# Kernel optimization log

Hardware: AMD Instinct MI355X
Metric: run time of the kernel (lower is better)

## Reference

```python
import jax, jax.numpy as jnp
import numpy as np

ALPHA = 0.1        # axis_aligned_projection threshold
NEG_INF = -1e30    # large negative used for masking (softmax-equivalent to -inf)


def axis_aligned_projection(x, alpha=ALPHA):
    x_abs = jnp.abs(x)
    max_vals = jnp.max(x_abs, axis=-1, keepdims=True)
    axis_weights = jnp.where(x_abs >= alpha * max_vals, x_abs, 0.0)
    return axis_weights * jnp.sign(x)


def setup_inputs() -> dict:
    key = jax.random.key(0)
    kq, kk, kv = jax.random.split(key, 3)
    B, L, H, E = 4, 2048, 8, 64
    S, D = L, E
    queries = jax.random.normal(kq, (B, L, H, E), dtype=jnp.float32)
    keys = jax.random.normal(kk, (B, S, H, E), dtype=jnp.float32)
    values = jax.random.normal(kv, (B, S, H, D), dtype=jnp.float32)
    # TriangularCausalMask: True strictly above the diagonal -> masked out
    causal = jnp.triu(jnp.ones((L, S), dtype=jnp.bool_), k=1)
    attn_mask = jnp.broadcast_to(causal[None, None], (B, 1, L, S))
    return {"queries": queries, "keys": keys, "values": values, "attn_mask": attn_mask}


def reference(queries, keys, values, attn_mask):
    B, L, H, E = queries.shape
    scale = 1.0 / jnp.sqrt(jnp.float32(E))
    q = axis_aligned_projection(queries)
    k = axis_aligned_projection(keys)
    # [B,H,L,S] dense scores (the module materializes the full matrix)
    scores = jnp.einsum('blhe,bshe->bhls', q, k)
    scores = jnp.where(attn_mask, NEG_INF, scores)
    A = jax.nn.softmax(scale * scores, axis=-1)  # dropout is identity in eval mode
    V = jnp.einsum('bhls,bshd->blhd', A, values)
    return V
```

## Files before the change

kernel.cpp:

```cpp
#include <hip/hip_runtime.h>
#include <hip/hip_bf16.h>
#include <stdint.h>

#define B_ 4
#define L_ 2048
#define H_ 8
#define E_ 64
#define ALPHA 0.1f
#define LOG2E 1.44269504088896f
#define QSCALE (0.125f * LOG2E)
#define KSTR 72

typedef float f32x4 __attribute__((ext_vector_type(4)));
typedef short bf16x8 __attribute__((ext_vector_type(8)));
typedef short bf16x4 __attribute__((ext_vector_type(4)));
typedef uint32_t u32;
typedef unsigned short u16;
typedef u32 u32x2 __attribute__((ext_vector_type(2)));

__device__ __forceinline__ u16 f2bf(float f) {
    u32 x = __builtin_bit_cast(u32, f);
    u32 r = x + 0x7fffu + ((x >> 16) & 1u);
    return (u16)(r >> 16);
}

__device__ __forceinline__ u32 pk2bf(float a, float b) {
    u32 ua = __builtin_bit_cast(u32, a) + 0x8000u;
    u32 ub = __builtin_bit_cast(u32, b) + 0x8000u;
    return (ua >> 16) | (ub & 0xffff0000u);
}

__device__ __forceinline__ f32x4 mfma16x16x16bf16(bf16x4 a, bf16x4 b, f32x4 c) {
#if __has_builtin(__builtin_amdgcn_mfma_f32_16x16x16bf16_1k)
    return __builtin_amdgcn_mfma_f32_16x16x16bf16_1k(a, b, c, 0, 0, 0);
#elif __has_builtin(__builtin_amdgcn_mfma_f32_16x16x16_bf16)
    return __builtin_amdgcn_mfma_f32_16x16x16_bf16(a, b, c, 0, 0, 0);
#else
    f32x4 d;
    asm volatile("v_mfma_f32_16x16x16_bf16 %0, %1, %2, %3"
                 : "=v"(d) : "v"(a), "v"(b), "v"(c));
    return d;
#endif
}

__device__ __forceinline__ void dma16(const u16* g, u16* l) {
    __builtin_amdgcn_global_load_lds(
        (const __attribute__((address_space(1))) void*)g,
        (__attribute__((address_space(3))) void*)l, 16, 0, 0);
}

__global__ __launch_bounds__(256) void prep_kernel(const float* __restrict__ qin,
                                                   const float* __restrict__ kin,
                                                   const float* __restrict__ vin,
                                                   u16* __restrict__ qp,
                                                   u16* __restrict__ kp,
                                                   u16* __restrict__ vt) {
    __shared__ u16 tile[64][66];
    if (blockIdx.x < 4096) {
        const int RG = (B_ * L_ * H_) / 8;
        int wave = threadIdx.x >> 6, lane = threadIdx.x & 63;
        int g = blockIdx.x * 4 + wave;
        const float* src;
        u16* dst;
        int gr, ostr;
        float sc;
        if (g < RG) { src = qin; dst = qp; gr = g; sc = QSCALE; ostr = 64; }
        else        { src = kin; dst = kp; gr = g - RG; sc = 1.0f; ostr = KSTR; }

        int rig = lane >> 3;
        int c = (lane & 7) * 4;
        int row = gr * 8 + rig;

        const float* rp = src + (size_t)row * 64;
        float4 v0 = *(const float4*)(rp + c);
        float4 v1 = *(const float4*)(rp + c + 32);
        float f[8] = {v0.x, v0.y, v0.z, v0.w, v1.x, v1.y, v1.z, v1.w};

        float mx = 0.f;
#pragma unroll
        for (int i = 0; i < 8; ++i) mx = fmaxf(mx, fabsf(f[i]));
#pragma unroll
        for (int m = 1; m < 8; m <<= 1) mx = fmaxf(mx, __shfl_xor(mx, m));
        float thr = ALPHA * mx;

        u16 o[8];
#pragma unroll
        for (int i = 0; i < 8; ++i)
            o[i] = (fabsf(f[i]) >= thr) ? f2bf(f[i] * sc) : (u16)0;

        int b = row >> 14;
        int l = (row >> 3) & (L_ - 1);
        int h = row & 7;
        u16* orow = dst + ((size_t)(b * H_ + h) * L_ + l) * ostr;
        uint2 p0 = {(u32)o[0] | ((u32)o[1] << 16), (u32)o[2] | ((u32)o[3] << 16)};
        uint2 p1 = {(u32)o[4] | ((u32)o[5] << 16), (u32)o[6] | ((u32)o[7] << 16)};
        *(uint2*)(orow + c) = p0;
        *(uint2*)(orow + c + 32) = p1;
    } else {
        int bx = blockIdx.x - 4096;
        int bh = bx >> 5, sblk = bx & 31;
        int b = bh >> 3, h = bh & 7;
        int t = threadIdx.x;
        int s0 = sblk * 64;

#pragma unroll
        for (int p = 0; p < 2; ++p) {
            int sl = p * 32 + (t >> 3);
            int c = (t & 7) * 4;
            const float* rp = vin + (((size_t)(b * L_ + s0 + sl)) * H_ + h) * 64;
            float4 a = *(const float4*)(rp + c);
            float4 bb = *(const float4*)(rp + c + 32);
            u32* d0 = (u32*)&tile[sl][c];
            d0[0] = (u32)f2bf(a.x) | ((u32)f2bf(a.y) << 16);
            d0[1] = (u32)f2bf(a.z) | ((u32)f2bf(a.w) << 16);
            u32* d1 = (u32*)&tile[sl][c + 32];
            d1[0] = (u32)f2bf(bb.x) | ((u32)f2bf(bb.y) << 16);
            d1[1] = (u32)f2bf(bb.z) | ((u32)f2bf(bb.w) << 16);
        }
        __syncthreads();
#pragma unroll
        for (int p = 0; p < 2; ++p) {
            int d = p * 32 + (t >> 3);
            int sc2 = (t & 7) * 8;
            u16 o[8];
#pragma unroll
            for (int i = 0; i < 8; ++i) o[i] = tile[sc2 + i][d];
            uint4 val;
            val.x = (u32)o[0] | ((u32)o[1] << 16);
            val.y = (u32)o[2] | ((u32)o[3] << 16);
            val.z = (u32)o[4] | ((u32)o[5] << 16);
            val.w = (u32)o[6] | ((u32)o[7] << 16);
            *(uint4*)(vt + ((size_t)(bh * 32 + sblk) * 64 + d) * KSTR + sc2) = val;
        }
    }
}

__global__ __launch_bounds__(256, 2) void flash_kernel(const u16* __restrict__ Qp,
                                                       const u16* __restrict__ Kp,
                                                       const u16* __restrict__ Vt,
                                                       float* __restrict__ out) {
    __shared__ u16 kbuf[2][64 * KSTR];
    __shared__ u16 vbuf[2][64 * KSTR];
    int t = threadIdx.x;
    int wave = t >> 6, lane = t & 63;
    int bh = blockIdx.x & 31;
    int j = blockIdx.x >> 5;
    int qg = (blockIdx.x < 256) ? (15 - j) : (j - 8);
    int lo = lane & 15, quad = lane >> 4;
    int b = bh >> 3, h = bh & 7;
    int qA = qg * 128 + wave * 16;
    int qB = qA + 64;
    int dA = qg * 2;
    int T = dA + 1;

    const u16* kTiles = Kp + (size_t)bh * L_ * KSTR;
    const u16* vTiles = Vt + (size_t)bh * 32 * 64 * KSTR;

    auto stage = [&](int sb, int buf) {
        const u16* kg = kTiles + (size_t)sb * KSTR;
        const u16* vg = vTiles + (size_t)(sb >> 6) * 64 * KSTR;
        u16* kl = kbuf[buf];
        u16* vl = vbuf[buf];
        for (int i = wave; i < 18; i += 4) {
            if (i < 9) dma16(kg + i * 512 + lane * 8, kl + i * 512);
            else       dma16(vg + (i - 9) * 512 + lane * 8, vl + (i - 9) * 512);
        }
    };

    const u16* qbA = Qp + ((size_t)bh * L_ + qA + lo) * 64 + quad * 8;
    bf16x8 aQA0 = *(const bf16x8*)(qbA);
    bf16x8 aQA1 = *(const bf16x8*)(qbA + 32);
    const u16* qbB = Qp + ((size_t)bh * L_ + qB + lo) * 64 + quad * 8;
    bf16x8 aQB0 = *(const bf16x8*)(qbB);
    bf16x8 aQB1 = *(const bf16x8*)(qbB + 32);

    f32x4 oA[4], oB[4];
#pragma unroll
    for (int ni = 0; ni < 4; ++ni) {
        oA[ni] = (f32x4){0.f, 0.f, 0.f, 0.f};
        oB[ni] = (f32x4){0.f, 0.f, 0.f, 0.f};
    }
    float lsA = 0.f, lsB = 0.f;

    auto frag_proc = [&](bf16x8 k0, bf16x8 k1, const bf16x4* vf,
                         bf16x8 fq0, bf16x8 fq1, f32x4* oacc, float& lsacc,
                         bool diag) {
        f32x4 S = {0.f, 0.f, 0.f, 0.f};
        S = __builtin_amdgcn_mfma_f32_16x16x32_bf16(k0, fq0, S, 0, 0, 0);
        S = __builtin_amdgcn_mfma_f32_16x16x32_bf16(k1, fq1, S, 0, 0, 0);
        float P[4];
#pragma unroll
        for (int r = 0; r < 4; ++r) {
            float e = __builtin_amdgcn_exp2f(S[r]);
            P[r] = (diag && (quad * 4 + r > lo)) ? 0.f : e;
        }
        lsacc += (P[0] + P[1]) + (P[2] + P[3]);
        u32x2 pk = {pk2bf(P[0], P[1]), pk2bf(P[2], P[3])};
        bf16x4 aP = __builtin_bit_cast(bf16x4, pk);
#pragma unroll
        for (int ni = 0; ni < 4; ++ni)
            oacc[ni] = mfma16x16x16bf16(aP, vf[ni], oacc[ni]);
    };

    stage(0, 0);
    __syncthreads();

    for (int kt = 0; kt < dA; ++kt) {
        int cur = kt & 1;
        stage((kt + 1) << 6, cur ^ 1);
        const u16* ks = kbuf[cur];
        const u16* vs = vbuf[cur];
#pragma unroll
        for (int sub = 0; sub < 4; ++sub) {
            bf16x8 k0 = *(const bf16x8*)(ks + (sub * 16 + lo) * KSTR + quad * 8);
            bf16x8 k1 = *(const bf16x8*)(ks + (sub * 16 + lo) * KSTR + 32 + quad * 8);
            bf16x4 vf[4];
#pragma unroll
            for (int ni = 0; ni < 4; ++ni)
                vf[ni] = *(const bf16x4*)(vs + (ni * 16 + lo) * KSTR + sub * 16 + quad * 4);
            frag_proc(k0, k1, vf, aQA0, aQA1, oA, lsA, false);
            frag_proc(k0, k1, vf, aQB0, aQB1, oB, lsB, false);
        }
        __syncthreads();
    }

    {
        int cur = dA & 1;
        stage(T << 6, cur ^ 1);
        const u16* ks = kbuf[cur];
        const u16* vs = vbuf[cur];
#pragma unroll
        for (int sub = 0; sub < 4; ++sub) {
            bf16x8 k0 = *(const bf16x8*)(ks + (sub * 16 + lo) * KSTR + quad * 8);
            bf16x8 k1 = *(const bf16x8*)(ks + (sub * 16 + lo) * KSTR + 32 + quad * 8);
            bf16x4 vf[4];
#pragma unroll
            for (int ni = 0; ni < 4; ++ni)
                vf[ni] = *(const bf16x4*)(vs + (ni * 16 + lo) * KSTR + sub * 16 + quad * 4);
            frag_proc(k0, k1, vf, aQB0, aQB1, oB, lsB, false);
            if (sub < wave)
                frag_proc(k0, k1, vf, aQA0, aQA1, oA, lsA, false);
            else if (sub == wave)
                frag_proc(k0, k1, vf, aQA0, aQA1, oA, lsA, true);
        }
        __syncthreads();
    }

    {
        int cur = T & 1;
        const u16* ks = kbuf[cur];
        const u16* vs = vbuf[cur];
        for (int sub = 0; sub <= wave; ++sub) {
            bf16x8 k0 = *(const bf16x8*)(ks + (sub * 16 + lo) * KSTR + quad * 8);
            bf16x8 k1 = *(const bf16x8*)(ks + (sub * 16 + lo) * KSTR + 32 + quad * 8);
            bf16x4 vf[4];
#pragma unroll
            for (int ni = 0; ni < 4; ++ni)
                vf[ni] = *(const bf16x4*)(vs + (ni * 16 + lo) * KSTR + sub * 16 + quad * 4);
            frag_proc(k0, k1, vf, aQB0, aQB1, oB, lsB, sub == wave);
        }
    }

    auto epi = [&](float ls, const f32x4* oacc, int q0f) {
        ls += __shfl_xor(ls, 16);
        ls += __shfl_xor(ls, 32);
#pragma unroll
        for (int r = 0; r < 4; ++r) {
            float lr = __shfl(ls, quad * 4 + r);
            float inv = 1.0f / lr;
            int q = q0f + quad * 4 + r;
            float* ob = out + (((size_t)(b * L_ + q)) * H_ + h) * 64 + lo;
            ob[0]  = oacc[0][r] * inv;
            ob[16] = oacc[1][r] * inv;
            ob[32] = oacc[2][r] * inv;
            ob[48] = oacc[3][r] * inv;
        }
    };
    epi(lsA, oA, qA);
    epi(lsB, oB, qB);
}

extern "C" void kernel_launch(void* const* d_in, const int* in_sizes, int n_in,
                              void* d_out, int out_size, void* d_ws, size_t ws_size,
                              hipStream_t stream) {
    const float* q = (const float*)d_in[0];
    const float* k = (const float*)d_in[1];
    const float* v = (const float*)d_in[2];
    float* out = (float*)d_out;

    const size_t QSZ = (size_t)B_ * H_ * L_ * 64;
    const size_t KSZ = (size_t)B_ * H_ * L_ * KSTR;
    u16* qp = (u16*)d_ws;
    u16* kp = qp + QSZ;
    u16* vt = kp + KSZ;

    prep_kernel<<<5120, 256, 0, stream>>>(q, k, v, qp, kp, vt);
    flash_kernel<<<512, 256, 0, stream>>>(qp, kp, vt, out);
}
```

Measured before the change: 172.9 us.

## Split 128-row query blocks into 64-row blocks and double grid size

Each block now handles 64 query rows (one 16-row fragment per wave) instead of two 16-row fragments per wave across 128 rows. The grid doubles to 1024 blocks, launch bounds rise to 4 blocks per CU, and the causal schedule is remapped so heavy and light blocks interleave. The aim is better occupancy and load balance. The cost is that each K/V tile staged in LDS is reused by half as many query rows, so LDS and global traffic go up.

```diff
diff --git a/kernel.cpp b/kernel.cpp
--- a/kernel.cpp
+++ b/kernel.cpp
@@ -135,7 +135,7 @@
     }
 }
 
-__global__ __launch_bounds__(256, 2) void flash_kernel(const u16* __restrict__ Qp,
+__global__ __launch_bounds__(256, 4) void flash_kernel(const u16* __restrict__ Qp,
                                                        const u16* __restrict__ Kp,
                                                        const u16* __restrict__ Vt,
                                                        float* __restrict__ out) {
@@ -144,14 +144,12 @@
     int t = threadIdx.x;
     int wave = t >> 6, lane = t & 63;
     int bh = blockIdx.x & 31;
-    int j = blockIdx.x >> 5;
-    int qg = (blockIdx.x < 256) ? (15 - j) : (j - 8);
+    int r5 = blockIdx.x >> 5;
+    int g = r5 & 7, kr = r5 >> 3;
+    int qq = (kr == 0) ? (31 - g) : (kr == 1) ? (16 + g) : (kr == 2) ? (15 - g) : g;
     int lo = lane & 15, quad = lane >> 4;
+    int q0 = qq * 64 + wave * 16;
     int b = bh >> 3, h = bh & 7;
-    int qA = qg * 128 + wave * 16;
-    int qB = qA + 64;
-    int dA = qg * 2;
-    int T = dA + 1;
 
     const u16* kTiles = Kp + (size_t)bh * L_ * KSTR;
     const u16* vTiles = Vt + (size_t)bh * 32 * 64 * KSTR;
@@ -167,117 +165,75 @@
         }
     };
 
-    const u16* qbA = Qp + ((size_t)bh * L_ + qA + lo) * 64 + quad * 8;
-    bf16x8 aQA0 = *(const bf16x8*)(qbA);
-    bf16x8 aQA1 = *(const bf16x8*)(qbA + 32);
-    const u16* qbB = Qp + ((size_t)bh * L_ + qB + lo) * 64 + quad * 8;
-    bf16x8 aQB0 = *(const bf16x8*)(qbB);
-    bf16x8 aQB1 = *(const bf16x8*)(qbB + 32);
-
-    f32x4 oA[4], oB[4];
-#pragma unroll
-    for (int ni = 0; ni < 4; ++ni) {
-        oA[ni] = (f32x4){0.f, 0.f, 0.f, 0.f};
-        oB[ni] = (f32x4){0.f, 0.f, 0.f, 0.f};
-    }
-    float lsA = 0.f, lsB = 0.f;
-
-    auto frag_proc = [&](bf16x8 k0, bf16x8 k1, const bf16x4* vf,
-                         bf16x8 fq0, bf16x8 fq1, f32x4* oacc, float& lsacc,
-                         bool diag) {
+    const u16* qbase = Qp + ((size_t)bh * L_ + q0 + lo) * 64 + quad * 8;
+    bf16x8 aQ0 = *(const bf16x8*)(qbase);
+    bf16x8 aQ1 = *(const bf16x8*)(qbase + 32);
+
+    f32x4 o[4];
+#pragma unroll
+    for (int ni = 0; ni < 4; ++ni) o[ni] = (f32x4){0.f, 0.f, 0.f, 0.f};
+    float ls = 0.f;
+
+    auto frag_proc = [&](const u16* ks, const u16* vs, int sub, bool diag) {
+        bf16x8 k0 = *(const bf16x8*)(ks + (sub * 16 + lo) * KSTR + quad * 8);
+        bf16x8 k1 = *(const bf16x8*)(ks + (sub * 16 + lo) * KSTR + 32 + quad * 8);
         f32x4 S = {0.f, 0.f, 0.f, 0.f};
-        S = __builtin_amdgcn_mfma_f32_16x16x32_bf16(k0, fq0, S, 0, 0, 0);
-        S = __builtin_amdgcn_mfma_f32_16x16x32_bf16(k1, fq1, S, 0, 0, 0);
+        S = __builtin_amdgcn_mfma_f32_16x16x32_bf16(k0, aQ0, S, 0, 0, 0);
+        S = __builtin_amdgcn_mfma_f32_16x16x32_bf16(k1, aQ1, S, 0, 0, 0);
+
+        bf16x4 vf[4];
+#pragma unroll
+        for (int ni = 0; ni < 4; ++ni)
+            vf[ni] = *(const bf16x4*)(vs + (ni * 16 + lo) * KSTR + sub * 16 + quad * 4);
+
         float P[4];
 #pragma unroll
         for (int r = 0; r < 4; ++r) {
             float e = __builtin_amdgcn_exp2f(S[r]);
             P[r] = (diag && (quad * 4 + r > lo)) ? 0.f : e;
         }
-        lsacc += (P[0] + P[1]) + (P[2] + P[3]);
+        ls += (P[0] + P[1]) + (P[2] + P[3]);
         u32x2 pk = {pk2bf(P[0], P[1]), pk2bf(P[2], P[3])};
         bf16x4 aP = __builtin_bit_cast(bf16x4, pk);
 #pragma unroll
         for (int ni = 0; ni < 4; ++ni)
-            oacc[ni] = mfma16x16x16bf16(aP, vf[ni], oacc[ni]);
+            o[ni] = mfma16x16x16bf16(aP, vf[ni], o[ni]);
     };
 
     stage(0, 0);
     __syncthreads();
 
-    for (int kt = 0; kt < dA; ++kt) {
+    for (int kt = 0; kt < qq; ++kt) {
         int cur = kt & 1;
         stage((kt + 1) << 6, cur ^ 1);
         const u16* ks = kbuf[cur];
         const u16* vs = vbuf[cur];
 #pragma unroll
-        for (int sub = 0; sub < 4; ++sub) {
-            bf16x8 k0 = *(const bf16x8*)(ks + (sub * 16 + lo) * KSTR + quad * 8);
-            bf16x8 k1 = *(const bf16x8*)(ks + (sub * 16 + lo) * KSTR + 32 + quad * 8);
-            bf16x4 vf[4];
-#pragma unroll
-            for (int ni = 0; ni < 4; ++ni)
-                vf[ni] = *(const bf16x4*)(vs + (ni * 16 + lo) * KSTR + sub * 16 + quad * 4);
-            frag_proc(k0, k1, vf, aQA0, aQA1, oA, lsA, false);
-            frag_proc(k0, k1, vf, aQB0, aQB1, oB, lsB, false);
-        }
+        for (int sub = 0; sub < 4; ++sub) frag_proc(ks, vs, sub, false);
         __syncthreads();
     }
 
     {
-        int cur = dA & 1;
-        stage(T << 6, cur ^ 1);
+        int cur = qq & 1;
         const u16* ks = kbuf[cur];
         const u16* vs = vbuf[cur];
-#pragma unroll
-        for (int sub = 0; sub < 4; ++sub) {
-            bf16x8 k0 = *(const bf16x8*)(ks + (sub * 16 + lo) * KSTR + quad * 8);
-            bf16x8 k1 = *(const bf16x8*)(ks + (sub * 16 + lo) * KSTR + 32 + quad * 8);
-            bf16x4 vf[4];
-#pragma unroll
-            for (int ni = 0; ni < 4; ++ni)
-                vf[ni] = *(const bf16x4*)(vs + (ni * 16 + lo) * KSTR + sub * 16 + quad * 4);
-            frag_proc(k0, k1, vf, aQB0, aQB1, oB, lsB, false);
-            if (sub < wave)
-                frag_proc(k0, k1, vf, aQA0, aQA1, oA, lsA, false);
-            else if (sub == wave)
-                frag_proc(k0, k1, vf, aQA0, aQA1, oA, lsA, true);
-        }
-        __syncthreads();
-    }
-
-    {
-        int cur = T & 1;
-        const u16* ks = kbuf[cur];
-        const u16* vs = vbuf[cur];
-        for (int sub = 0; sub <= wave; ++sub) {
-            bf16x8 k0 = *(const bf16x8*)(ks + (sub * 16 + lo) * KSTR + quad * 8);
-            bf16x8 k1 = *(const bf16x8*)(ks + (sub * 16 + lo) * KSTR + 32 + quad * 8);
-            bf16x4 vf[4];
-#pragma unroll
-            for (int ni = 0; ni < 4; ++ni)
-                vf[ni] = *(const bf16x4*)(vs + (ni * 16 + lo) * KSTR + sub * 16 + quad * 4);
-            frag_proc(k0, k1, vf, aQB0, aQB1, oB, lsB, sub == wave);
-        }
-    }
-
-    auto epi = [&](float ls, const f32x4* oacc, int q0f) {
-        ls += __shfl_xor(ls, 16);
-        ls += __shfl_xor(ls, 32);
-#pragma unroll
-        for (int r = 0; r < 4; ++r) {
-            float lr = __shfl(ls, quad * 4 + r);
-            float inv = 1.0f / lr;
-            int q = q0f + quad * 4 + r;
-            float* ob = out + (((size_t)(b * L_ + q)) * H_ + h) * 64 + lo;
-            ob[0]  = oacc[0][r] * inv;
-            ob[16] = oacc[1][r] * inv;
-            ob[32] = oacc[2][r] * inv;
-            ob[48] = oacc[3][r] * inv;
-        }
-    };
-    epi(lsA, oA, qA);
-    epi(lsB, oB, qB);
+        for (int sub = 0; sub < wave; ++sub) frag_proc(ks, vs, sub, false);
+        frag_proc(ks, vs, wave, true);
+    }
+
+    ls += __shfl_xor(ls, 16);
+    ls += __shfl_xor(ls, 32);
+#pragma unroll
+    for (int r = 0; r < 4; ++r) {
+        float lr = __shfl(ls, quad * 4 + r);
+        float inv = 1.0f / lr;
+        int q = q0 + quad * 4 + r;
+        float* ob = out + (((size_t)(b * L_ + q)) * H_ + h) * 64 + lo;
+        ob[0]  = o[0][r] * inv;
+        ob[16] = o[1][r] * inv;
+        ob[32] = o[2][r] * inv;
+        ob[48] = o[3][r] * inv;
+    }
 }
 
 extern "C" void kernel_launch(void* const* d_in, const int* in_sizes, int n_in,
@@ -295,5 +251,5 @@
     u16* vt = kp + KSZ;
 
     prep_kernel<<<5120, 256, 0, stream>>>(q, k, v, qp, kp, vt);
-    flash_kernel<<<512, 256, 0, stream>>>(qp, kp, vt, out);
-}
+    flash_kernel<<<1024, 256, 0, stream>>>(qp, kp, vt, out);
+}
```

Result: faster. 168.3 us (-2.7%).

## Pair mirrored query tiles per block for balanced causal workload

Applied to the files above, without the earlier changes.

Each block now processes query tile j together with its mirror tile 31-j, instead of two adjacent 64-row tiles of one 128-row group. This makes the causal work per block constant, which removes the load imbalance across blocks. It also drops the separate diagonal-tile section and moves the A-tile diagonal masking into the main loop as branches. Those branches inside the inner loop may add divergence or instruction overhead.

```diff
diff --git a/kernel.cpp b/kernel.cpp
--- a/kernel.cpp
+++ b/kernel.cpp
@@ -144,14 +144,14 @@
     int t = threadIdx.x;
     int wave = t >> 6, lane = t & 63;
     int bh = blockIdx.x & 31;
-    int j = blockIdx.x >> 5;
-    int qg = (blockIdx.x < 256) ? (15 - j) : (j - 8);
+    int jj = blockIdx.x >> 5;
+    int j = (jj < 8) ? jj : (23 - jj);
     int lo = lane & 15, quad = lane >> 4;
     int b = bh >> 3, h = bh & 7;
-    int qA = qg * 128 + wave * 16;
-    int qB = qA + 64;
-    int dA = qg * 2;
-    int T = dA + 1;
+    int qqA = j;
+    int qqB = 31 - j;
+    int qA = qqA * 64 + wave * 16;
+    int qB = qqB * 64 + wave * 16;
 
     const u16* kTiles = Kp + (size_t)bh * L_ * KSTR;
     const u16* vTiles = Vt + (size_t)bh * 32 * 64 * KSTR;
@@ -205,7 +205,7 @@
     stage(0, 0);
     __syncthreads();
 
-    for (int kt = 0; kt < dA; ++kt) {
+    for (int kt = 0; kt < qqB; ++kt) {
         int cur = kt & 1;
         stage((kt + 1) << 6, cur ^ 1);
         const u16* ks = kbuf[cur];
@@ -218,36 +218,21 @@
 #pragma unroll
             for (int ni = 0; ni < 4; ++ni)
                 vf[ni] = *(const bf16x4*)(vs + (ni * 16 + lo) * KSTR + sub * 16 + quad * 4);
-            frag_proc(k0, k1, vf, aQA0, aQA1, oA, lsA, false);
             frag_proc(k0, k1, vf, aQB0, aQB1, oB, lsB, false);
+            if (kt < qqA) {
+                frag_proc(k0, k1, vf, aQA0, aQA1, oA, lsA, false);
+            } else if (kt == qqA) {
+                if (sub < wave)
+                    frag_proc(k0, k1, vf, aQA0, aQA1, oA, lsA, false);
+                else if (sub == wave)
+                    frag_proc(k0, k1, vf, aQA0, aQA1, oA, lsA, true);
+            }
         }
         __syncthreads();
     }
 
     {
-        int cur = dA & 1;
-        stage(T << 6, cur ^ 1);
-        const u16* ks = kbuf[cur];
-        const u16* vs = vbuf[cur];
-#pragma unroll
-        for (int sub = 0; sub < 4; ++sub) {
-            bf16x8 k0 = *(const bf16x8*)(ks + (sub * 16 + lo) * KSTR + quad * 8);
-            bf16x8 k1 = *(const bf16x8*)(ks + (sub * 16 + lo) * KSTR + 32 + quad * 8);
-            bf16x4 vf[4];
-#pragma unroll
-            for (int ni = 0; ni < 4; ++ni)
-                vf[ni] = *(const bf16x4*)(vs + (ni * 16 + lo) * KSTR + sub * 16 + quad * 4);
-            frag_proc(k0, k1, vf, aQB0, aQB1, oB, lsB, false);
-            if (sub < wave)
-                frag_proc(k0, k1, vf, aQA0, aQA1, oA, lsA, false);
-            else if (sub == wave)
-                frag_proc(k0, k1, vf, aQA0, aQA1, oA, lsA, true);
-        }
-        __syncthreads();
-    }
-
-    {
-        int cur = T & 1;
+        int cur = qqB & 1;
         const u16* ks = kbuf[cur];
         const u16* vs = vbuf[cur];
         for (int sub = 0; sub <= wave; ++sub) {
```

Measured after the change: 174.9 us. Within noise of the previous version (+1.1%).
